# Kernel tuning notes

Hardware: AMD Instinct MI355X
Metric: run time of the kernel (lower is better)

The kernel has to match this reference:

```python
import jax, jax.numpy as jnp
import numpy as np

N = 1024       # nodes
D1 = 64        # hidden_dim_1
D2 = 64        # hidden_dim_2
E = 16384      # edges
P = 8192       # query pairs
MAXX = 100     # max node label -> Embedding(MAXX+1, D1)
EPS = 1e-5     # LayerNorm eps (no affine)


def _ln(t):
    m = jnp.mean(t, axis=-1, keepdims=True)
    v = jnp.mean((t - m) ** 2, axis=-1, keepdims=True)
    return (t - m) / jnp.sqrt(v + EPS)


def setup_inputs() -> dict:
    key = jax.random.key(0)
    ks = jax.random.split(key, 12)
    s = 0.1
    x = jax.random.randint(ks[0], (N,), 0, MAXX + 1)
    ei = jax.random.randint(ks[1], (2, E), 0, N)
    pos = jax.random.randint(ks[2], (P, 2), 0, N)
    emb = jax.random.normal(ks[3], (MAXX + 1, D1)) * s
    sage_Wl = jax.random.normal(ks[4], (2, D1, D1)) * s   # lin_l weight (aggr path, has bias)
    sage_bl = jnp.zeros((2, D1))
    sage_Wr = jax.random.normal(ks[5], (2, D1, D1)) * s   # lin_r weight (root path, no bias)
    h_W = jax.random.normal(ks[6], (D1 + 1, D2)) * s
    h_b = jnp.zeros((D2,))
    g_W = jax.random.normal(ks[7], (D1 + 1 + 2 * D2, D2)) * s
    g_b = jnp.zeros((D2,))
    lin_W = jax.random.normal(ks[8], (D2, 1)) * s
    lin_b = jnp.zeros((1,))
    return {"x": x, "ei": ei, "pos": pos, "emb": emb,
            "sage_Wl": sage_Wl, "sage_bl": sage_bl, "sage_Wr": sage_Wr,
            "h_W": h_W, "h_b": h_b, "g_W": g_W, "g_b": g_b,
            "lin_W": lin_W, "lin_b": lin_b}


def reference(x, ei, pos, emb, sage_Wl, sage_bl, sage_Wr, h_W, h_b, g_W, g_b, lin_W, lin_b):
    n = N
    src, dst = ei[0], ei[1]
    h = emb[x]                                            # (n, D1)
    # SAGEConv x2: mean-aggregate src->dst, lin_l(aggr)+bias + lin_r(root); then LN (no affine, no relu)
    deg = jax.ops.segment_sum(jnp.ones((E,), h.dtype), dst, num_segments=n)
    deg = jnp.maximum(deg, 1.0)[:, None]
    for i in range(2):
        aggr = jax.ops.segment_sum(h[src], dst, num_segments=n) / deg
        h = _ln(aggr @ sage_Wl[i] + sage_bl[i] + h @ sage_Wr[i])
    # pairwise outer product features: (n, n, D1)
    A = h[:, None, :] * h[None, :, :]
    eim = jnp.zeros((n * n,), h.dtype).at[src * n + dst].set(1.0).reshape(n, n, 1)
    A = jnp.concatenate([A, eim], axis=-1)                # (n, n, D1+1)
    # mataggr: B = h_1(A); row/col sums; D = cat(A, vec_p, vec_q); g_1(D)
    B = jax.nn.relu(_ln(A @ h_W + h_b))                   # (n, n, D2)
    vec_p = jnp.sum(B, axis=1, keepdims=True)             # (n, 1, D2)
    vec_q = jnp.sum(B, axis=0, keepdims=True)             # (1, n, D2)
    Dm = jnp.concatenate([A,
                          jnp.broadcast_to(vec_p, (n, n, D2)),
                          jnp.broadcast_to(vec_q, (n, n, D2))], axis=-1)
    G = jax.nn.relu(_ln(Dm @ g_W + g_b))                  # (n, n, D2)
    # symmetrize and gather query pairs
    S = (G * jnp.transpose(G, (1, 0, 2))).reshape(n * n, D2)
    sel = S[pos[:, 0] * n + pos[:, 1]]                    # (P, D2)
    return sel @ lin_W + lin_b                            # (P, 1)
```

## Files before the change

### kernel.cpp

```cpp
#include <hip/hip_runtime.h>
#include <hip/hip_bf16.h>

#define NN 1024
#define DD 64
#define EE 16384
#define PP 8192
#define EPSF 1e-5f
#define SWP (DD + 8)

typedef __hip_bfloat16 bf16;
typedef __attribute__((ext_vector_type(8))) short short8;
typedef __attribute__((ext_vector_type(4))) float f32x4;

static __device__ __forceinline__ float dec1(const void* src, int i, int fl) {
    if (fl) return ((const float*)src)[i];
    return __bfloat162float(((const bf16*)src)[i]);
}
static __device__ __forceinline__ unsigned short f2bf_u(float f) {
    bf16 h = __float2bfloat16(f);
    return *reinterpret_cast<unsigned short*>(&h);
}
static __device__ __forceinline__ float bfu2f(unsigned short u) {
    return __uint_as_float(((unsigned int)u) << 16);
}
static __device__ __forceinline__ int probe_fl(const void* emb) {
    int lane = threadIdx.x & 63;
    unsigned short raw = ((const unsigned short*)emb)[lane];
    float v = __uint_as_float(((unsigned int)raw) << 16);
    return (__ballot(!(fabsf(v) <= 1e3f)) != 0ull) ? 1 : 0;
}

__global__ __launch_bounds__(1024) void k_prep(
        const void* __restrict__ emb, const void* __restrict__ sWl,
        const void* __restrict__ sbl, const void* __restrict__ sWr,
        const void* __restrict__ hW, const void* __restrict__ hb,
        const void* __restrict__ gW, const void* __restrict__ gb,
        const void* __restrict__ lW, const void* __restrict__ lb,
        const int* __restrict__ x, const int* __restrict__ ei,
        float* __restrict__ Wlf, float* __restrict__ blf, float* __restrict__ Wrf,
        float* __restrict__ WfT, float* __restrict__ hbw,
        float* __restrict__ gWf, float* __restrict__ linf,
        unsigned short* __restrict__ gWbfT,
        float* __restrict__ h0,
        unsigned int* __restrict__ eim, unsigned int* __restrict__ eimT,
        int* __restrict__ rowptr, int* __restrict__ csrc) {
    __shared__ int sdeg[NN];
    __shared__ int stmp[1024];
    const int b = blockIdx.x, tid = threadIdx.x;
    const int fl = probe_fl(emb);

    if (b < 97) {
        const int vb = b * 4 + (tid >> 8);
        const int vt = tid & 255;
        if (vb < 256) {
            int z = vb * 256 + vt;
            if (z < 32768) eim[z] = 0u;
            else           eimT[z - 32768] = 0u;
        }
        if (vb < 32) { int i = vb * 256 + vt; Wlf[i] = dec1(sWl, i, fl); }
        else if (vb == 32) { if (vt < 128) blf[vt] = dec1(sbl, vt, fl); }
        else if (vb < 65) { int i = (vb - 33) * 256 + vt; Wrf[i] = dec1(sWr, i, fl); }
        else if (vb < 82) {
            int i = (vb - 65) * 256 + vt;
            if (i < 4096) { int n = i >> 6, k = i & 63; WfT[n * DD + k] = dec1(hW, k * DD + n, fl); }
            else if (i < 4160) hbw[i - 4096] = dec1(hb, i - 4096, fl);
            else if (i < 4224) hbw[64 + (i - 4160)] = dec1(hW, 64 * DD + (i - 4160), fl);
        } else if (vb < 131) {
            int i = (vb - 82) * 256 + vt;
            if (i < 193 * DD) gWf[i] = dec1(gW, i, fl);
            else if (i < 194 * DD) gWf[i] = dec1(gb, i - 193 * DD, fl);
        } else if (vb == 131) {
            if (vt < DD) linf[vt] = dec1(lW, vt, fl);
            else if (vt == DD) linf[DD] = dec1(lb, 0, fl);
#pragma unroll
            for (int u = 0; u < 16; ++u) {
                int i = vt * 16 + u;
                int m = i >> 6, k = i & 63;
                gWbfT[i] = f2bf_u(dec1(gW, k * DD + m, fl));
            }
        } else if (vb < 388) {
            int i = (vb - 132) * 256 + vt;
            int node = i >> 6, f = i & 63;
            h0[i] = dec1(emb, x[node] * DD + f, fl);
        }
    } else {
        sdeg[tid] = 0;
        __syncthreads();
        for (int base = 0; base < EE; base += 8192) {
            int d8[8];
#pragma unroll
            for (int u = 0; u < 8; ++u) d8[u] = ei[EE + base + u * 1024 + tid];
#pragma unroll
            for (int u = 0; u < 8; ++u) atomicAdd(&sdeg[d8[u]], 1);
        }
        __syncthreads();
        int v = sdeg[tid];
        stmp[tid] = v;
        __syncthreads();
        for (int off = 1; off < 1024; off <<= 1) {
            int a = (tid >= off) ? stmp[tid - off] : 0;
            __syncthreads();
            stmp[tid] += a;
            __syncthreads();
        }
        int excl = stmp[tid] - v;
        rowptr[tid] = excl;
        sdeg[tid] = excl;
        if (tid == 1023) rowptr[NN] = stmp[1023];
        __syncthreads();
        for (int base = 0; base < EE; base += 8192) {
            int d8[8], s8[8];
#pragma unroll
            for (int u = 0; u < 8; ++u) {
                d8[u] = ei[EE + base + u * 1024 + tid];
                s8[u] = ei[base + u * 1024 + tid];
            }
#pragma unroll
            for (int u = 0; u < 8; ++u) {
                int c = atomicAdd(&sdeg[d8[u]], 1);
                csrc[c] = s8[u];
            }
        }
    }
}

static __device__ __forceinline__ void sage_core(
        const float* sWl, const float* sWr, float* sa, float* sh,
        int node, int lane,
        const int* __restrict__ rowptr, const int* __restrict__ csrc,
        const float* __restrict__ hin, const void* __restrict__ sbl, int boff, int fl,
        float* __restrict__ hout, unsigned short* __restrict__ hbf) {
    int r0 = rowptr[node], r1 = rowptr[node + 1];
    float s = 0.f;
    int r = r0;
    for (; r + 4 <= r1; r += 4) {
        int i0 = csrc[r], i1 = csrc[r + 1], i2 = csrc[r + 2], i3 = csrc[r + 3];
        float v0 = hin[i0 * DD + lane], v1 = hin[i1 * DD + lane];
        float v2 = hin[i2 * DD + lane], v3 = hin[i3 * DD + lane];
        s += (v0 + v1) + (v2 + v3);
    }
    for (; r < r1; ++r) s += hin[csrc[r] * DD + lane];
    sa[lane] = s / (float)max(r1 - r0, 1);
    sh[lane] = hin[node * DD + lane];
    float o = dec1(sbl, boff + lane, fl);
    for (int k = 0; k < DD; ++k)
        o += sa[k] * sWl[k * DD + lane] + sh[k] * sWr[k * DD + lane];
    float m = o;
    for (int off = 32; off; off >>= 1) m += __shfl_xor(m, off);
    m *= (1.f / DD);
    float d0 = o - m;
    float v = d0 * d0;
    for (int off = 32; off; off >>= 1) v += __shfl_xor(v, off);
    v *= (1.f / DD);
    float rr = d0 * rsqrtf(v + EPSF);
    hout[node * DD + lane] = rr;
    if (hbf) hbf[node * DD + lane] = f2bf_u(rr);
}

__global__ __launch_bounds__(256) void k_sage0(
        const void* __restrict__ emb, const int* __restrict__ ei,
        const int* __restrict__ rowptr, const int* __restrict__ csrc,
        const float* __restrict__ h0,
        const float* __restrict__ Wlf, const void* __restrict__ sbl,
        const float* __restrict__ Wrf,
        float* __restrict__ h1,
        unsigned int* __restrict__ eim, unsigned int* __restrict__ eimT) {
    __shared__ __align__(16) float sWl[DD * DD];
    __shared__ __align__(16) float sWr[DD * DD];
    __shared__ float sa4[4 * DD], sh4[4 * DD];
    const int b = blockIdx.x, tid = threadIdx.x;
    const int lane = tid & 63, wave = tid >> 6;
    const int fl = probe_fl(emb);
    for (int i = tid * 4; i < DD * DD; i += 1024) {
        *(float4*)(sWl + i) = *(const float4*)(Wlf + i);
        *(float4*)(sWr + i) = *(const float4*)(Wrf + i);
    }
    if (tid < 64) {
        int e = b * 64 + tid;
        int s = ei[e], d = ei[EE + e];
        unsigned int idx = (unsigned int)(s * NN + d);
        atomicOr(&eim[idx >> 5], 1u << (idx & 31));
        unsigned int idxT = (unsigned int)(d * NN + s);
        atomicOr(&eimT[idxT >> 5], 1u << (idxT & 31));
    }
    __syncthreads();
    sage_core(sWl, sWr, sa4 + wave * DD, sh4 + wave * DD, b * 4 + wave, lane,
              rowptr, csrc, h0, sbl, 0, fl, h1, (unsigned short*)nullptr);
}

__global__ __launch_bounds__(256) void k_sage1(
        const void* __restrict__ emb,
        const int* __restrict__ rowptr, const int* __restrict__ csrc,
        const float* __restrict__ h1,
        const float* __restrict__ Wlf, const void* __restrict__ sbl,
        const float* __restrict__ Wrf,
        float* __restrict__ h2, unsigned short* __restrict__ hbf) {
    __shared__ __align__(16) float sWl[DD * DD];
    __shared__ __align__(16) float sWr[DD * DD];
    __shared__ float sa4[4 * DD], sh4[4 * DD];
    const int b = blockIdx.x, tid = threadIdx.x;
    const int lane = tid & 63, wave = tid >> 6;
    const int fl = probe_fl(emb);
    for (int i = tid * 4; i < DD * DD; i += 1024) {
        *(float4*)(sWl + i) = *(const float4*)(Wlf + DD * DD + i);
        *(float4*)(sWr + i) = *(const float4*)(Wrf + DD * DD + i);
    }
    __syncthreads();
    sage_core(sWl, sWr, sa4 + wave * DD, sh4 + wave * DD, b * 4 + wave, lane,
              rowptr, csrc, h1, sbl, DD, fl, h2, hbf);
}

__global__ __launch_bounds__(256) void k_bstage(
        const float* __restrict__ h2, const unsigned short* __restrict__ hbf,
        const float* __restrict__ WfT, const float* __restrict__ hbw,
        const unsigned int* __restrict__ eim, const unsigned int* __restrict__ eimT,
        const float* __restrict__ gWf,
        float* __restrict__ ppb, float* __restrict__ qqb) {
    __shared__ __align__(16) unsigned short sW[DD * SWP];
    __shared__ __align__(16) float red[4 * 128];
    __shared__ float swc[2];
    const int b = blockIdx.x, tid = threadIdx.x;
    const int lane = tid & 63, wave = tid >> 6;
    const int l15 = lane & 15, quad = lane >> 4;

    {
        int m = tid >> 2;
        int k0 = (tid & 3) * 16;
        const float* hi = h2 + b * DD;
        const float* wr = WfT + m * DD;
        unsigned short tmp[16];
#pragma unroll
        for (int u = 0; u < 16; ++u) tmp[u] = f2bf_u(hi[k0 + u] * wr[k0 + u]);
        *(short8*)(sW + m * SWP + k0) = *(short8*)tmp;
        *(short8*)(sW + m * SWP + k0 + 8) = *(short8*)(tmp + 8);
    }
    if (wave == 0) {
        float wv = hbw[64 + lane];
        float s = wv, s2 = wv * wv;
        for (int off = 32; off; off >>= 1) {
            s += __shfl_xor(s, off);
            s2 += __shfl_xor(s2, off);
        }
        if (lane == 0) { swc[0] = s; swc[1] = s2; }
    }
    __syncthreads();
    const float SW = swc[0], SWW = swc[1];

    short8 Af[4][2];
#pragma unroll
    for (int mt = 0; mt < 4; ++mt)
#pragma unroll
        for (int kt = 0; kt < 2; ++kt)
            Af[mt][kt] = *(const short8*)(sW + (mt * 16 + l15) * SWP + kt * 32 + quad * 8);

    f32x4 hb04[4], hww4[4];
#pragma unroll
    for (int mt = 0; mt < 4; ++mt) {
        hb04[mt] = *(const f32x4*)(hbw + mt * 16 + quad * 4);
        hww4[mt] = *(const f32x4*)(hbw + 64 + mt * 16 + quad * 4);
    }

    f32x4 accf[4], accb[4];
#pragma unroll
    for (int mt = 0; mt < 4; ++mt) {
        accf[mt] = (f32x4){0.f, 0.f, 0.f, 0.f};
        accb[mt] = (f32x4){0.f, 0.f, 0.f, 0.f};
    }

    const unsigned short* pB = hbf + (wave * 16 + l15) * DD + quad * 8;
    const unsigned int* pF = eim + b * 32 + (wave >> 1);
    const unsigned int* pBk = eimT + b * 32 + (wave >> 1);
    const int shft = (wave & 1) * 16;

    short8 B0 = *(const short8*)(pB);
    short8 B1 = *(const short8*)(pB + 32);
    pB += 4096;
    unsigned int wfC = pF[0], wbC = pBk[0];
    pF += 2; pBk += 2;

    for (int it = 0; it < 16; ++it) {
        short8 cB0 = B0, cB1 = B1;
        B0 = *(const short8*)(pB);
        B1 = *(const short8*)(pB + 32);
        pB += 4096;
        unsigned int sf = (wfC >> shft) & 0xFFFFu;
        unsigned int sb = (wbC >> shft) & 0xFFFFu;
        wfC = pF[0]; wbC = pBk[0];
        pF += 2; pBk += 2;

        f32x4 C[4];
#pragma unroll
        for (int mt = 0; mt < 4; ++mt) C[mt] = hb04[mt];
#pragma unroll
        for (int mt = 0; mt < 4; ++mt)
            C[mt] = __builtin_amdgcn_mfma_f32_16x16x32_bf16(Af[mt][0], cB0, C[mt], 0, 0, 0);
#pragma unroll
        for (int mt = 0; mt < 4; ++mt)
            C[mt] = __builtin_amdgcn_mfma_f32_16x16x32_bf16(Af[mt][1], cB1, C[mt], 0, 0, 0);

        float ef = (float)((sf >> l15) & 1u);
        f32x4 efv = {ef, ef, ef, ef};
        f32x4 s1a = {0.f, 0.f, 0.f, 0.f}, s2a = {0.f, 0.f, 0.f, 0.f};
#pragma unroll
        for (int mt = 0; mt < 4; ++mt) {
            C[mt] += efv * hww4[mt];
            s1a += C[mt];
            s2a += C[mt] * C[mt];
        }
        float s1 = (s1a.x + s1a.y) + (s1a.z + s1a.w);
        float s2 = (s2a.x + s2a.y) + (s2a.z + s2a.w);
        s1 += __shfl_xor(s1, 16); s1 += __shfl_xor(s1, 32);
        s2 += __shfl_xor(s2, 16); s2 += __shfl_xor(s2, 32);
        float mean = s1 * (1.f / DD);
        float var = fmaxf(s2 * (1.f / DD) - mean * mean, 0.f);
        float rs = rsqrtf(var + EPSF);
        float mrs = mean * rs;
        f32x4 rsv = {rs, rs, rs, rs}, mrsv = {mrs, mrs, mrs, mrs};
        f32x4 zero = {0.f, 0.f, 0.f, 0.f};

        if (sf == sb) {
#pragma unroll
            for (int mt = 0; mt < 4; ++mt) {
                f32x4 u = __builtin_elementwise_max(C[mt] * rsv - mrsv, zero);
                accf[mt] += u;
                accb[mt] += u;
            }
        } else {
#pragma unroll
            for (int mt = 0; mt < 4; ++mt)
                accf[mt] += __builtin_elementwise_max(C[mt] * rsv - mrsv, zero);
            float de = (float)((sb >> l15) & 1u) - ef;
            f32x4 dva = {0.f, 0.f, 0.f, 0.f};
#pragma unroll
            for (int mt = 0; mt < 4; ++mt) dva += C[mt] * hww4[mt];
            float dot = (dva.x + dva.y) + (dva.z + dva.w);
            dot += __shfl_xor(dot, 16); dot += __shfl_xor(dot, 32);
            float t1 = s1 + de * SW;
            float t2 = s2 + 2.f * de * dot + de * de * SWW;
            float mean2 = t1 * (1.f / DD);
            float var2 = fmaxf(t2 * (1.f / DD) - mean2 * mean2, 0.f);
            float rs2 = rsqrtf(var2 + EPSF);
            float mrs2 = mean2 * rs2;
            float drs = de * rs2;
            f32x4 rs2v = {rs2, rs2, rs2, rs2};
            f32x4 mrs2v = {mrs2, mrs2, mrs2, mrs2};
            f32x4 drsv = {drs, drs, drs, drs};
#pragma unroll
            for (int mt = 0; mt < 4; ++mt) {
                f32x4 th = mrs2v - drsv * hww4[mt];
                accb[mt] += __builtin_elementwise_max(C[mt] * rs2v - th, zero);
            }
        }
    }

    float af[4][4], ab[4][4];
#pragma unroll
    for (int mt = 0; mt < 4; ++mt)
#pragma unroll
        for (int r = 0; r < 4; ++r) { af[mt][r] = accf[mt][r]; ab[mt][r] = accb[mt][r]; }
#pragma unroll
    for (int step = 1; step < 16; step <<= 1)
#pragma unroll
        for (int mt = 0; mt < 4; ++mt)
#pragma unroll
            for (int r = 0; r < 4; ++r) {
                af[mt][r] += __shfl_xor(af[mt][r], step);
                ab[mt][r] += __shfl_xor(ab[mt][r], step);
            }
    if (l15 == 0) {
#pragma unroll
        for (int mt = 0; mt < 4; ++mt)
#pragma unroll
            for (int r = 0; r < 4; ++r) {
                int m = mt * 16 + quad * 4 + r;
                red[wave * 128 + m] = af[mt][r];
                red[wave * 128 + DD + m] = ab[mt][r];
            }
    }
    __syncthreads();
    if (tid < 128) {
        float sum = red[tid] + red[128 + tid] + red[256 + tid] + red[384 + tid];
        red[tid] = sum;
    }
    __syncthreads();
    if (wave < 2) {
        const float* sv = red + wave * DD;
        int row0 = wave ? 129 : 65;
        float o = 0.f;
        for (int k = 0; k < DD; ++k) o += sv[k] * gWf[(row0 + k) * DD + lane];
        (wave ? qqb : ppb)[b * DD + lane] = o;
    }
}

__global__ __launch_bounds__(128) void k_final(
        const void* __restrict__ emb,
        const int* __restrict__ pos, const unsigned short* __restrict__ hbf,
        const float* __restrict__ gWf, const unsigned short* __restrict__ gWbfT,
        const unsigned int* __restrict__ eim,
        const float* __restrict__ ppb, const float* __restrict__ qqb,
        const float* __restrict__ linf, void* __restrict__ outv) {
    const int b = blockIdx.x, tid = threadIdx.x;
    const int lane = tid & 63, wave = tid >> 6;
    const int l15 = lane & 15, quad = lane >> 4;
    const int fl = probe_fl(emb);

    short8 A0f[4], A1f[4];
#pragma unroll
    for (int mt = 0; mt < 4; ++mt) {
        A0f[mt] = *(const short8*)(gWbfT + (mt * 16 + l15) * DD + quad * 8);
        A1f[mt] = *(const short8*)(gWbfT + (mt * 16 + l15) * DD + 32 + quad * 8);
    }

    int pp_ = b * 32 + wave * 16 + l15;
    int a = pos[2 * pp_], bb = pos[2 * pp_ + 1];
    short8 ha0 = *(const short8*)(hbf + a * DD + quad * 8);
    short8 hb0v = *(const short8*)(hbf + bb * DD + quad * 8);
    short8 ha1 = *(const short8*)(hbf + a * DD + 32 + quad * 8);
    short8 hb1v = *(const short8*)(hbf + bb * DD + 32 + quad * 8);
    short8 B0, B1;
#pragma unroll
    for (int j = 0; j < 8; ++j) {
        B0[j] = (short)f2bf_u(bfu2f((unsigned short)ha0[j]) * bfu2f((unsigned short)hb0v[j]));
        B1[j] = (short)f2bf_u(bfu2f((unsigned short)ha1[j]) * bfu2f((unsigned short)hb1v[j]));
    }

    f32x4 C[4];
#pragma unroll
    for (int mt = 0; mt < 4; ++mt) C[mt] = (f32x4){0.f, 0.f, 0.f, 0.f};
#pragma unroll
    for (int mt = 0; mt < 4; ++mt)
        C[mt] = __builtin_amdgcn_mfma_f32_16x16x32_bf16(A0f[mt], B0, C[mt], 0, 0, 0);
#pragma unroll
    for (int mt = 0; mt < 4; ++mt)
        C[mt] = __builtin_amdgcn_mfma_f32_16x16x32_bf16(A1f[mt], B1, C[mt], 0, 0, 0);

    unsigned int iab = (unsigned int)(a * NN + bb), iba = (unsigned int)(bb * NN + a);
    float eab = (float)((eim[iab >> 5] >> (iab & 31)) & 1u);
    float eba = (float)((eim[iba >> 5] >> (iba & 31)) & 1u);

    float u1[4][4], u2[4][4];
    float s1 = 0.f, s12 = 0.f, s2 = 0.f, s22 = 0.f;
#pragma unroll
    for (int mt = 0; mt < 4; ++mt) {
        int m0 = mt * 16 + quad * 4;
        f32x4 w64v = *(const f32x4*)(gWf + 64 * DD + m0);
        f32x4 gbv  = *(const f32x4*)(gWf + 193 * DD + m0);
        f32x4 ppa  = *(const f32x4*)(ppb + a * DD + m0);
        f32x4 qqb_ = *(const f32x4*)(qqb + bb * DD + m0);
        f32x4 ppb_ = *(const f32x4*)(ppb + bb * DD + m0);
        f32x4 qqa  = *(const f32x4*)(qqb + a * DD + m0);
#pragma unroll
        for (int r = 0; r < 4; ++r) {
            float v1 = C[mt][r] + eab * w64v[r] + ppa[r] + qqb_[r] + gbv[r];
            float v2 = C[mt][r] + eba * w64v[r] + ppb_[r] + qqa[r] + gbv[r];
            u1[mt][r] = v1; u2[mt][r] = v2;
            s1 += v1; s12 += v1 * v1;
            s2 += v2; s22 += v2 * v2;
        }
    }
    s1 += __shfl_xor(s1, 16);  s1 += __shfl_xor(s1, 32);
    s12 += __shfl_xor(s12, 16); s12 += __shfl_xor(s12, 32);
    s2 += __shfl_xor(s2, 16);  s2 += __shfl_xor(s2, 32);
    s22 += __shfl_xor(s22, 16); s22 += __shfl_xor(s22, 32);
    float mean1 = s1 * (1.f / DD);
    float rs1 = rsqrtf(fmaxf(s12 * (1.f / DD) - mean1 * mean1, 0.f) + EPSF);
    float mrs1 = mean1 * rs1;
    float mean2 = s2 * (1.f / DD);
    float rs2 = rsqrtf(fmaxf(s22 * (1.f / DD) - mean2 * mean2, 0.f) + EPSF);
    float mrs2 = mean2 * rs2;

    float r = 0.f;
#pragma unroll
    for (int mt = 0; mt < 4; ++mt) {
        f32x4 lw = *(const f32x4*)(linf + mt * 16 + quad * 4);
#pragma unroll
        for (int rr = 0; rr < 4; ++rr) {
            float g1 = fmaxf(u1[mt][rr] * rs1 - mrs1, 0.f);
            float g2 = fmaxf(u2[mt][rr] * rs2 - mrs2, 0.f);
            r += g1 * g2 * lw[rr];
        }
    }
    r += __shfl_xor(r, 16); r += __shfl_xor(r, 32);
    if (quad == 0) {
        float res = r + linf[DD];
        if (fl) ((float*)outv)[pp_] = res;
        else    ((bf16*)outv)[pp_] = __float2bfloat16(res);
    }
}

extern "C" void kernel_launch(void* const* d_in, const int* in_sizes, int n_in,
                              void* d_out, int out_size, void* d_ws, size_t ws_size,
                              hipStream_t stream) {
    const int* x   = (const int*)d_in[0];
    const int* ei  = (const int*)d_in[1];
    const int* pos = (const int*)d_in[2];
    const void* emb = d_in[3];

    char* w = (char*)d_ws;
    auto alloc = [&](size_t bytes) {
        void* q = (void*)w;
        w += (bytes + 255) & ~(size_t)255;
        return q;
    };
    unsigned int* eim  = (unsigned int*)alloc(NN * NN / 8);
    unsigned int* eimT = (unsigned int*)alloc(NN * NN / 8);
    float* h0   = (float*)alloc(NN * DD * 4);
    float* h1   = (float*)alloc(NN * DD * 4);
    float* h2   = (float*)alloc(NN * DD * 4);
    unsigned short* hbf = (unsigned short*)alloc(NN * DD * 2 + 8192);
    float* Wlf  = (float*)alloc(2 * DD * DD * 4);
    float* blf  = (float*)alloc(2 * DD * 4);
    float* Wrf  = (float*)alloc(2 * DD * DD * 4);
    float* WfT  = (float*)alloc(DD * DD * 4);
    float* hbw  = (float*)alloc(128 * 4);
    float* gWf  = (float*)alloc(194 * DD * 4);
    float* linf = (float*)alloc(65 * 4);
    unsigned short* gWbfT = (unsigned short*)alloc(DD * DD * 2);
    float* ppb  = (float*)alloc(NN * DD * 4);
    float* qqb  = (float*)alloc(NN * DD * 4);
    int* rowptr = (int*)alloc((NN + 1) * 4);
    int* csrc   = (int*)alloc(EE * 4);

    k_prep<<<98, 1024, 0, stream>>>(emb, d_in[4], d_in[5], d_in[6], d_in[7], d_in[8],
                                    d_in[9], d_in[10], d_in[11], d_in[12],
                                    x, ei, Wlf, blf, Wrf, WfT, hbw, gWf, linf, gWbfT,
                                    h0, eim, eimT, rowptr, csrc);
    k_sage0<<<256, 256, 0, stream>>>(emb, ei, rowptr, csrc, h0, Wlf, d_in[5], Wrf,
                                     h1, eim, eimT);
    k_sage1<<<256, 256, 0, stream>>>(emb, rowptr, csrc, h1, Wlf, d_in[5], Wrf, h2, hbf);
    k_bstage<<<NN, 256, 0, stream>>>(h2, hbf, WfT, hbw, eim, eimT, gWf, ppb, qqb);
    k_final<<<PP / 32, 128, 0, stream>>>(emb, pos, hbf, gWf, gWbfT, eim, ppb, qqb, linf, d_out);
}
```

Baseline: 145.2 us.

## Fuse prep and two SAGE layers into one kernel with grid barriers

Merges the prep, sage0 and sage1 kernels into a single 256-block, 1024-thread kernel that separates stages with a software grid barrier built on a global atomic counter. The aim is to remove two kernel launch gaps and their serialization overhead. It also skips the edge-indicator bias add in the B-stage MFMA loop when a tile has no edges, and feeds the bias straight in as the MFMA accumulator. The grid barrier relies on all 256 blocks being co-resident, which is a deadlock risk. Only 256 of the 1024 threads do the SAGE work, and the larger shared memory footprint lowers occupancy.

```diff
diff --git a/kernel.cpp b/kernel.cpp
--- a/kernel.cpp
+++ b/kernel.cpp
@@ -30,98 +30,18 @@
     return (__ballot(!(fabsf(v) <= 1e3f)) != 0ull) ? 1 : 0;
 }
 
-__global__ __launch_bounds__(1024) void k_prep(
-        const void* __restrict__ emb, const void* __restrict__ sWl,
-        const void* __restrict__ sbl, const void* __restrict__ sWr,
-        const void* __restrict__ hW, const void* __restrict__ hb,
-        const void* __restrict__ gW, const void* __restrict__ gb,
-        const void* __restrict__ lW, const void* __restrict__ lb,
-        const int* __restrict__ x, const int* __restrict__ ei,
-        float* __restrict__ Wlf, float* __restrict__ blf, float* __restrict__ Wrf,
-        float* __restrict__ WfT, float* __restrict__ hbw,
-        float* __restrict__ gWf, float* __restrict__ linf,
-        unsigned short* __restrict__ gWbfT,
-        float* __restrict__ h0,
-        unsigned int* __restrict__ eim, unsigned int* __restrict__ eimT,
-        int* __restrict__ rowptr, int* __restrict__ csrc) {
-    __shared__ int sdeg[NN];
-    __shared__ int stmp[1024];
-    const int b = blockIdx.x, tid = threadIdx.x;
-    const int fl = probe_fl(emb);
-
-    if (b < 97) {
-        const int vb = b * 4 + (tid >> 8);
-        const int vt = tid & 255;
-        if (vb < 256) {
-            int z = vb * 256 + vt;
-            if (z < 32768) eim[z] = 0u;
-            else           eimT[z - 32768] = 0u;
-        }
-        if (vb < 32) { int i = vb * 256 + vt; Wlf[i] = dec1(sWl, i, fl); }
-        else if (vb == 32) { if (vt < 128) blf[vt] = dec1(sbl, vt, fl); }
-        else if (vb < 65) { int i = (vb - 33) * 256 + vt; Wrf[i] = dec1(sWr, i, fl); }
-        else if (vb < 82) {
-            int i = (vb - 65) * 256 + vt;
-            if (i < 4096) { int n = i >> 6, k = i & 63; WfT[n * DD + k] = dec1(hW, k * DD + n, fl); }
-            else if (i < 4160) hbw[i - 4096] = dec1(hb, i - 4096, fl);
-            else if (i < 4224) hbw[64 + (i - 4160)] = dec1(hW, 64 * DD + (i - 4160), fl);
-        } else if (vb < 131) {
-            int i = (vb - 82) * 256 + vt;
-            if (i < 193 * DD) gWf[i] = dec1(gW, i, fl);
-            else if (i < 194 * DD) gWf[i] = dec1(gb, i - 193 * DD, fl);
-        } else if (vb == 131) {
-            if (vt < DD) linf[vt] = dec1(lW, vt, fl);
-            else if (vt == DD) linf[DD] = dec1(lb, 0, fl);
-#pragma unroll
-            for (int u = 0; u < 16; ++u) {
-                int i = vt * 16 + u;
-                int m = i >> 6, k = i & 63;
-                gWbfT[i] = f2bf_u(dec1(gW, k * DD + m, fl));
-            }
-        } else if (vb < 388) {
-            int i = (vb - 132) * 256 + vt;
-            int node = i >> 6, f = i & 63;
-            h0[i] = dec1(emb, x[node] * DD + f, fl);
-        }
-    } else {
-        sdeg[tid] = 0;
-        __syncthreads();
-        for (int base = 0; base < EE; base += 8192) {
-            int d8[8];
-#pragma unroll
-            for (int u = 0; u < 8; ++u) d8[u] = ei[EE + base + u * 1024 + tid];
-#pragma unroll
-            for (int u = 0; u < 8; ++u) atomicAdd(&sdeg[d8[u]], 1);
-        }
-        __syncthreads();
-        int v = sdeg[tid];
-        stmp[tid] = v;
-        __syncthreads();
-        for (int off = 1; off < 1024; off <<= 1) {
-            int a = (tid >= off) ? stmp[tid - off] : 0;
-            __syncthreads();
-            stmp[tid] += a;
-            __syncthreads();
-        }
-        int excl = stmp[tid] - v;
-        rowptr[tid] = excl;
-        sdeg[tid] = excl;
-        if (tid == 1023) rowptr[NN] = stmp[1023];
-        __syncthreads();
-        for (int base = 0; base < EE; base += 8192) {
-            int d8[8], s8[8];
-#pragma unroll
-            for (int u = 0; u < 8; ++u) {
-                d8[u] = ei[EE + base + u * 1024 + tid];
-                s8[u] = ei[base + u * 1024 + tid];
-            }
-#pragma unroll
-            for (int u = 0; u < 8; ++u) {
-                int c = atomicAdd(&sdeg[d8[u]], 1);
-                csrc[c] = s8[u];
-            }
-        }
-    }
+__device__ unsigned int g_bar;
+
+static __device__ __forceinline__ void gsync(unsigned int target) {
+    __syncthreads();
+    if (threadIdx.x == 0) {
+        __threadfence();
+        __hip_atomic_fetch_add(&g_bar, 1u, __ATOMIC_ACQ_REL, __HIP_MEMORY_SCOPE_AGENT);
+        while (__hip_atomic_load(&g_bar, __ATOMIC_RELAXED, __HIP_MEMORY_SCOPE_AGENT) < target)
+            __builtin_amdgcn_s_sleep(2);
+        __threadfence();
+    }
+    __syncthreads();
 }
 
 static __device__ __forceinline__ void sage_core(
@@ -157,21 +77,110 @@
     if (hbf) hbf[node * DD + lane] = f2bf_u(rr);
 }
 
-__global__ __launch_bounds__(256) void k_sage0(
-        const void* __restrict__ emb, const int* __restrict__ ei,
-        const int* __restrict__ rowptr, const int* __restrict__ csrc,
-        const float* __restrict__ h0,
-        const float* __restrict__ Wlf, const void* __restrict__ sbl,
-        const float* __restrict__ Wrf,
-        float* __restrict__ h1,
-        unsigned int* __restrict__ eim, unsigned int* __restrict__ eimT) {
+__global__ __launch_bounds__(1024) void k_fused(
+        const void* __restrict__ emb, const void* __restrict__ sWl_in,
+        const void* __restrict__ sbl, const void* __restrict__ sWr_in,
+        const void* __restrict__ hW, const void* __restrict__ hb,
+        const void* __restrict__ gW, const void* __restrict__ gb,
+        const void* __restrict__ lW, const void* __restrict__ lb,
+        const int* __restrict__ x, const int* __restrict__ ei,
+        float* __restrict__ Wlf, float* __restrict__ blf, float* __restrict__ Wrf,
+        float* __restrict__ WfT, float* __restrict__ hbw,
+        float* __restrict__ gWf, float* __restrict__ linf,
+        unsigned short* __restrict__ gWbfT,
+        float* __restrict__ h0,
+        unsigned int* __restrict__ eim, unsigned int* __restrict__ eimT,
+        int* __restrict__ rowptr, int* __restrict__ csrc,
+        float* __restrict__ h1, float* __restrict__ h2,
+        unsigned short* __restrict__ hbf) {
+    __shared__ int sdeg[NN];
+    __shared__ int stmp[1024];
     __shared__ __align__(16) float sWl[DD * DD];
     __shared__ __align__(16) float sWr[DD * DD];
     __shared__ float sa4[4 * DD], sh4[4 * DD];
     const int b = blockIdx.x, tid = threadIdx.x;
     const int lane = tid & 63, wave = tid >> 6;
     const int fl = probe_fl(emb);
-    for (int i = tid * 4; i < DD * DD; i += 1024) {
+    const unsigned int gbase =
+        (__hip_atomic_load(&g_bar, __ATOMIC_RELAXED, __HIP_MEMORY_SCOPE_AGENT) / 512u) * 512u;
+
+    if (b < 97) {
+        const int vb = b * 4 + (tid >> 8);
+        const int vt = tid & 255;
+        if (vb < 256) {
+            int z = vb * 256 + vt;
+            if (z < 32768) eim[z] = 0u;
+            else           eimT[z - 32768] = 0u;
+        }
+        if (vb < 32) { int i = vb * 256 + vt; Wlf[i] = dec1(sWl_in, i, fl); }
+        else if (vb == 32) { if (vt < 128) blf[vt] = dec1(sbl, vt, fl); }
+        else if (vb < 65) { int i = (vb - 33) * 256 + vt; Wrf[i] = dec1(sWr_in, i, fl); }
+        else if (vb < 82) {
+            int i = (vb - 65) * 256 + vt;
+            if (i < 4096) { int n = i >> 6, k = i & 63; WfT[n * DD + k] = dec1(hW, k * DD + n, fl); }
+            else if (i < 4160) hbw[i - 4096] = dec1(hb, i - 4096, fl);
+            else if (i < 4224) hbw[64 + (i - 4160)] = dec1(hW, 64 * DD + (i - 4160), fl);
+        } else if (vb < 131) {
+            int i = (vb - 82) * 256 + vt;
+            if (i < 193 * DD) gWf[i] = dec1(gW, i, fl);
+            else if (i < 194 * DD) gWf[i] = dec1(gb, i - 193 * DD, fl);
+        } else if (vb == 131) {
+            if (vt < DD) linf[vt] = dec1(lW, vt, fl);
+            else if (vt == DD) linf[DD] = dec1(lb, 0, fl);
+#pragma unroll
+            for (int u = 0; u < 16; ++u) {
+                int i = vt * 16 + u;
+                int m = i >> 6, k = i & 63;
+                gWbfT[i] = f2bf_u(dec1(gW, k * DD + m, fl));
+            }
+        } else if (vb < 388) {
+            int i = (vb - 132) * 256 + vt;
+            int node = i >> 6, f = i & 63;
+            h0[i] = dec1(emb, x[node] * DD + f, fl);
+        }
+    } else if (b == 97) {
+        sdeg[tid] = 0;
+        __syncthreads();
+        for (int base = 0; base < EE; base += 8192) {
+            int d8[8];
+#pragma unroll
+            for (int u = 0; u < 8; ++u) d8[u] = ei[EE + base + u * 1024 + tid];
+#pragma unroll
+            for (int u = 0; u < 8; ++u) atomicAdd(&sdeg[d8[u]], 1);
+        }
+        __syncthreads();
+        int v = sdeg[tid];
+        stmp[tid] = v;
+        __syncthreads();
+        for (int off = 1; off < 1024; off <<= 1) {
+            int a = (tid >= off) ? stmp[tid - off] : 0;
+            __syncthreads();
+            stmp[tid] += a;
+            __syncthreads();
+        }
+        int excl = stmp[tid] - v;
+        rowptr[tid] = excl;
+        sdeg[tid] = excl;
+        if (tid == 1023) rowptr[NN] = stmp[1023];
+        __syncthreads();
+        for (int base = 0; base < EE; base += 8192) {
+            int d8[8], s8[8];
+#pragma unroll
+            for (int u = 0; u < 8; ++u) {
+                d8[u] = ei[EE + base + u * 1024 + tid];
+                s8[u] = ei[base + u * 1024 + tid];
+            }
+#pragma unroll
+            for (int u = 0; u < 8; ++u) {
+                int c = atomicAdd(&sdeg[d8[u]], 1);
+                csrc[c] = s8[u];
+            }
+        }
+    }
+
+    gsync(gbase + 256u);
+
+    for (int i = tid * 4; i < DD * DD; i += 4096) {
         *(float4*)(sWl + i) = *(const float4*)(Wlf + i);
         *(float4*)(sWr + i) = *(const float4*)(Wrf + i);
     }
@@ -184,30 +193,20 @@
         atomicOr(&eimT[idxT >> 5], 1u << (idxT & 31));
     }
     __syncthreads();
-    sage_core(sWl, sWr, sa4 + wave * DD, sh4 + wave * DD, b * 4 + wave, lane,
-              rowptr, csrc, h0, sbl, 0, fl, h1, (unsigned short*)nullptr);
-}
-
-__global__ __launch_bounds__(256) void k_sage1(
-        const void* __restrict__ emb,
-        const int* __restrict__ rowptr, const int* __restrict__ csrc,
-        const float* __restrict__ h1,
-        const float* __restrict__ Wlf, const void* __restrict__ sbl,
-        const float* __restrict__ Wrf,
-        float* __restrict__ h2, unsigned short* __restrict__ hbf) {
-    __shared__ __align__(16) float sWl[DD * DD];
-    __shared__ __align__(16) float sWr[DD * DD];
-    __shared__ float sa4[4 * DD], sh4[4 * DD];
-    const int b = blockIdx.x, tid = threadIdx.x;
-    const int lane = tid & 63, wave = tid >> 6;
-    const int fl = probe_fl(emb);
-    for (int i = tid * 4; i < DD * DD; i += 1024) {
+    if (tid < 256)
+        sage_core(sWl, sWr, sa4 + wave * DD, sh4 + wave * DD, b * 4 + wave, lane,
+                  rowptr, csrc, h0, sbl, 0, fl, h1, (unsigned short*)nullptr);
+
+    gsync(gbase + 512u);
+
+    for (int i = tid * 4; i < DD * DD; i += 4096) {
         *(float4*)(sWl + i) = *(const float4*)(Wlf + DD * DD + i);
         *(float4*)(sWr + i) = *(const float4*)(Wrf + DD * DD + i);
     }
     __syncthreads();
-    sage_core(sWl, sWr, sa4 + wave * DD, sh4 + wave * DD, b * 4 + wave, lane,
-              rowptr, csrc, h1, sbl, DD, fl, h2, hbf);
+    if (tid < 256)
+        sage_core(sWl, sWr, sa4 + wave * DD, sh4 + wave * DD, b * 4 + wave, lane,
+                  rowptr, csrc, h1, sbl, DD, fl, h2, hbf);
 }
 
 __global__ __launch_bounds__(256) void k_bstage(
@@ -290,20 +289,23 @@
 
         f32x4 C[4];
 #pragma unroll
-        for (int mt = 0; mt < 4; ++mt) C[mt] = hb04[mt];
-#pragma unroll
         for (int mt = 0; mt < 4; ++mt)
-            C[mt] = __builtin_amdgcn_mfma_f32_16x16x32_bf16(Af[mt][0], cB0, C[mt], 0, 0, 0);
+            C[mt] = __builtin_amdgcn_mfma_f32_16x16x32_bf16(Af[mt][0], cB0, hb04[mt], 0, 0, 0);
 #pragma unroll
         for (int mt = 0; mt < 4; ++mt)
             C[mt] = __builtin_amdgcn_mfma_f32_16x16x32_bf16(Af[mt][1], cB1, C[mt], 0, 0, 0);
 
-        float ef = (float)((sf >> l15) & 1u);
-        f32x4 efv = {ef, ef, ef, ef};
+        float ef = 0.f;
+        if ((sf | sb) != 0u) {
+            ef = (float)((sf >> l15) & 1u);
+            f32x4 efv = {ef, ef, ef, ef};
+#pragma unroll
+            for (int mt = 0; mt < 4; ++mt) C[mt] += efv * hww4[mt];
+        }
+
         f32x4 s1a = {0.f, 0.f, 0.f, 0.f}, s2a = {0.f, 0.f, 0.f, 0.f};
 #pragma unroll
         for (int mt = 0; mt < 4; ++mt) {
-            C[mt] += efv * hww4[mt];
             s1a += C[mt];
             s2a += C[mt] * C[mt];
         }
@@ -521,13 +523,10 @@
     int* rowptr = (int*)alloc((NN + 1) * 4);
     int* csrc   = (int*)alloc(EE * 4);
 
-    k_prep<<<98, 1024, 0, stream>>>(emb, d_in[4], d_in[5], d_in[6], d_in[7], d_in[8],
-                                    d_in[9], d_in[10], d_in[11], d_in[12],
-                                    x, ei, Wlf, blf, Wrf, WfT, hbw, gWf, linf, gWbfT,
-                                    h0, eim, eimT, rowptr, csrc);
-    k_sage0<<<256, 256, 0, stream>>>(emb, ei, rowptr, csrc, h0, Wlf, d_in[5], Wrf,
-                                     h1, eim, eimT);
-    k_sage1<<<256, 256, 0, stream>>>(emb, rowptr, csrc, h1, Wlf, d_in[5], Wrf, h2, hbf);
+    k_fused<<<256, 1024, 0, stream>>>(emb, d_in[4], d_in[5], d_in[6], d_in[7], d_in[8],
+                                      d_in[9], d_in[10], d_in[11], d_in[12],
+                                      x, ei, Wlf, blf, Wrf, WfT, hbw, gWf, linf, gWbfT,
+                                      h0, eim, eimT, rowptr, csrc, h1, h2, hbf);
     k_bstage<<<NN, 256, 0, stream>>>(h2, hbf, WfT, hbw, eim, eimT, gWf, ppb, qqb);
     k_final<<<PP / 32, 128, 0, stream>>>(emb, pos, hbf, gWf, gWbfT, eim, ppb, qqb, linf, d_out);
 }
```

Result: slower. 173.7 us (+19.6%).
